# Performance work log

Measured on AMD Instinct MI355X. Metric: run time of the kernel, lower is better.

Reference implementation:

```python
import math
import jax, jax.numpy as jnp
import numpy as np

B, L, N, D = 256, 50, 100000, 128

def _make_pe(max_len, d_model):
    # matches torch PositionalEncoding buffer (sin/cos scaled by 1/1000)
    pe = np.zeros((max_len, d_model), dtype=np.float32)
    position = np.arange(max_len, dtype=np.float32)[:, None]
    div_term = np.exp(np.arange(0, d_model, 2, dtype=np.float32) * (-math.log(10000.0) / d_model))
    pe[:, 0::2] = np.sin(position * div_term) / 1000.0
    pe[:, 1::2] = np.cos(position * div_term) / 1000.0
    return jnp.asarray(pe)

def setup_inputs() -> dict:
    key = jax.random.key(0)
    ks = jax.random.split(key, 8)
    g = 1.414  # xavier gain used in the torch module
    seeds = jax.random.randint(ks[0], (B, L), 0, N)
    labels = jax.random.randint(ks[1], (B,), 0, N)
    E = jax.random.normal(ks[2], (N, D), dtype=jnp.float32) * 0.02
    W1 = jax.random.normal(ks[3], (D, D), dtype=jnp.float32) * (g * math.sqrt(2.0 / (D + D)))
    W2 = jax.random.normal(ks[4], (D, D), dtype=jnp.float32) * (g * math.sqrt(2.0 / (D + D)))
    q = jax.random.normal(ks[5], (D,), dtype=jnp.float32) * (g * math.sqrt(2.0 / (1 + D)))
    b_att = jax.random.normal(ks[6], (1,), dtype=jnp.float32) * 0.01
    out_bias = jax.random.normal(ks[7], (N,), dtype=jnp.float32) * 0.01
    pe = _make_pe(L, D)
    return {"seeds": seeds, "labels": labels, "E": E, "W1": W1, "W2": W2,
            "q": q, "b_att": b_att, "out_bias": out_bias, "pe": pe}

def reference(seeds, labels, E, W1, W2, q, b_att, out_bias, pe):
    # user_representation: gather seed embeddings, add positional encoding (eval mode: dropout is identity)
    v = E[seeds] + pe[None, :, :]                 # (B, L, D)
    vn = v[:, -1, :]                              # (B, D) last element of each seed set
    # SoftAttention: att_i = q @ (W1 @ v_i + W2 @ vn + b); no softmax in original
    inp = jnp.einsum('bld,ed->ble', v, W1) + jnp.einsum('bd,ed->be', vn, W2)[:, None, :] + b_att[0]
    att = jnp.einsum('ble,e->bl', inp, q)         # (B, L) raw attention weights
    u = jnp.einsum('bl,bld->bd', att, v)          # (B, D) user representations
    # scores = F.linear(u, E, out_bias)
    scores = u @ E.T + out_bias                   # (B, N)
    logp = jax.nn.log_softmax(scores, axis=-1)
    base_loss = -jnp.mean(jnp.take_along_axis(logp, labels[:, None], axis=1))
    return scores, base_loss
```

## Files before the change

kernel.cpp:

```cpp
#include <hip/hip_runtime.h>
#include <hip/hip_bf16.h>

#define B_SZ 256
#define L_SZ 50
#define N_SZ 100000
#define D_SZ 128
#define NBT ((N_SZ + 63) / 64)

typedef __attribute__((ext_vector_type(8))) short bf16x8;
typedef __attribute__((ext_vector_type(4))) float f32x4;

__device__ inline unsigned short f2bf(float f) {
    union { float f; unsigned u; } v; v.f = f;
    unsigned r = v.u + 0x7FFFu + ((v.u >> 16) & 1u);
    return (unsigned short)(r >> 16);
}

__global__ __launch_bounds__(128) void k_ub(const int* __restrict__ seeds,
                                            const float* __restrict__ E,
                                            const float* __restrict__ pe,
                                            const float* __restrict__ W1,
                                            const float* __restrict__ W2,
                                            const float* __restrict__ q,
                                            const float* __restrict__ b_att,
                                            unsigned short* __restrict__ u_bf,
                                            float* __restrict__ loss_slot) {
    __shared__ float vbuf[L_SZ][D_SZ + 1];
    __shared__ float att[L_SZ];
    __shared__ float qs[D_SZ], qw1s[D_SZ], qw2s[D_SZ];
    __shared__ float c2s, qsums;
    int b = blockIdx.x, d = threadIdx.x;
    qs[d] = q[d];

    for (int l = 0; l < L_SZ; ++l) {
        int s = seeds[b * L_SZ + l];
        vbuf[l][d] = E[(size_t)s * D_SZ + d] + pe[l * D_SZ + d];
    }
    __syncthreads();

    float a1 = 0.f, a2 = 0.f;
    #pragma unroll 4
    for (int e = 0; e < D_SZ; ++e) {
        float qe = qs[e];
        a1 += qe * W1[e * D_SZ + d];
        a2 += qe * W2[e * D_SZ + d];
    }
    qw1s[d] = a1;
    qw2s[d] = a2;
    __syncthreads();

    if (d < L_SZ) {
        float acc = 0.f;
        #pragma unroll 4
        for (int k = 0; k < D_SZ; ++k) acc += vbuf[d][k] * qw1s[k];
        att[d] = acc;
    } else if (d == L_SZ) {
        float acc = 0.f;
        #pragma unroll 4
        for (int k = 0; k < D_SZ; ++k) acc += vbuf[L_SZ - 1][k] * qw2s[k];
        c2s = acc;
    } else if (d == L_SZ + 1) {
        float s = 0.f;
        for (int i = 0; i < D_SZ; ++i) s += qs[i];
        qsums = s;
    }
    __syncthreads();

    float add = c2s + b_att[0] * qsums;
    float u = 0.f;
    #pragma unroll 5
    for (int l = 0; l < L_SZ; ++l) u += (att[l] + add) * vbuf[l][d];
    u_bf[b * D_SZ + d] = f2bf(u);

    if (b == 0 && d == 0) loss_slot[0] = 0.f;
}

__global__ __launch_bounds__(256, 4) void k_gemm(const float* __restrict__ E,
                                                 const float* __restrict__ out_bias,
                                                 const unsigned short* __restrict__ u_bf,
                                                 float* __restrict__ scores,
                                                 float* __restrict__ partial) {
    __shared__ unsigned short us[128 * D_SZ];
    __shared__ float lds_sum[128];
    int tid = threadIdx.x;
    int w = tid >> 6, lane = tid & 63;
    int tile = blockIdx.x >> 1, hf = blockIdx.x & 1;
    if (tid < 128) lds_sum[tid] = 0.f;

    const char* ub = (const char*)u_bf + hf * 32768;
    #pragma unroll
    for (int r = 0; r < 8; ++r) {
        int off = r * 4096 + tid * 16;
        int b = off >> 8, inrow = off & 255;
        bf16x8 v = *(const bf16x8*)(ub + off);
        *(bf16x8*)((char*)us + b * 256 + (inrow ^ ((b & 7) << 4))) = v;
    }

    int nc = tile * 64 + w * 16;
    bool valid = (nc < N_SZ);
    int lo = lane & 15, hi = lane >> 4;
    int kb = hi * 8;

    long erow = valid ? (nc + lo) : 0;
    bf16x8 efrag[4];
    #pragma unroll
    for (int ks = 0; ks < 4; ++ks) {
        const float* p = E + (size_t)erow * D_SZ + ks * 32 + kb;
        float4 x = *(const float4*)p;
        float4 y = *(const float4*)(p + 4);
        bf16x8 f;
        f[0] = (short)f2bf(x.x); f[1] = (short)f2bf(x.y);
        f[2] = (short)f2bf(x.z); f[3] = (short)f2bf(x.w);
        f[4] = (short)f2bf(y.x); f[5] = (short)f2bf(y.y);
        f[6] = (short)f2bf(y.z); f[7] = (short)f2bf(y.w);
        efrag[ks] = f;
    }
    int nb = valid ? (nc + hi * 4) : 0;
    float4 bias4 = *(const float4*)(out_bias + nb);

    __syncthreads();

    #pragma unroll
    for (int rs = 0; rs < 8; ++rs) {
        f32x4 acc = (f32x4){0.f, 0.f, 0.f, 0.f};
        #pragma unroll
        for (int ks = 0; ks < 4; ++ks) {
            int b = rs * 16 + lo;
            int kcol = ks * 64 + hi * 16;
            bf16x8 uf = *(const bf16x8*)((const char*)us + b * 256 + (kcol ^ ((b & 7) << 4)));
            acc = __builtin_amdgcn_mfma_f32_16x16x32_bf16(efrag[ks], uf, acc, 0, 0, 0);
        }
        int jl = rs * 16 + lo;
        int jr = hf * 128 + jl;
        f32x4 c;
        c[0] = acc[0] + bias4.x;
        c[1] = acc[1] + bias4.y;
        c[2] = acc[2] + bias4.z;
        c[3] = acc[3] + bias4.w;
        if (valid)
            *(f32x4*)(scores + (size_t)jr * N_SZ + nb) = c;
        float p = __expf(c[0]) + __expf(c[1]) + __expf(c[2]) + __expf(c[3]);
        p += __shfl_xor(p, 16);
        p += __shfl_xor(p, 32);
        if (valid && hi == 0) atomicAdd(&lds_sum[jl], p);
    }
    __syncthreads();
    if (tid < 128) partial[(size_t)tile * B_SZ + hf * 128 + tid] = lds_sum[tid];
}

__global__ __launch_bounds__(256) void k_loss(const float* __restrict__ partial,
                                              const float* __restrict__ scores,
                                              const int* __restrict__ labels,
                                              float* __restrict__ out_loss) {
    int b = blockIdx.x, t = threadIdx.x;
    float acc = 0.f;
    for (int i = t; i < NBT; i += 256) acc += partial[(size_t)i * B_SZ + b];
    __shared__ float red[256];
    red[t] = acc;
    __syncthreads();
    for (int s = 128; s > 0; s >>= 1) {
        if (t < s) red[t] += red[t + s];
        __syncthreads();
    }
    if (t == 0) {
        int lab = labels[b];
        float val = scores[(size_t)b * N_SZ + lab] - logf(red[0]);
        atomicAdd(out_loss, -val * (1.0f / (float)B_SZ));
    }
}

extern "C" void kernel_launch(void* const* d_in, const int* in_sizes, int n_in,
                              void* d_out, int out_size, void* d_ws, size_t ws_size,
                              hipStream_t stream) {
    const int*   seeds    = (const int*)d_in[0];
    const int*   labels   = (const int*)d_in[1];
    const float* E        = (const float*)d_in[2];
    const float* W1       = (const float*)d_in[3];
    const float* W2       = (const float*)d_in[4];
    const float* q        = (const float*)d_in[5];
    const float* b_att    = (const float*)d_in[6];
    const float* out_bias = (const float*)d_in[7];
    const float* pe       = (const float*)d_in[8];

    float* scores = (float*)d_out;
    float* loss   = scores + (size_t)B_SZ * N_SZ;

    unsigned short* u_bf    = (unsigned short*)((char*)d_ws + 2048);
    float*          partial = (float*)((char*)d_ws + 67584);

    k_ub<<<B_SZ, 128, 0, stream>>>(seeds, E, pe, W1, W2, q, b_att, u_bf, loss);
    k_gemm<<<NBT * 2, 256, 0, stream>>>(E, out_bias, u_bf, scores, partial);
    k_loss<<<B_SZ, 256, 0, stream>>>(partial, scores, labels, loss);
}
```

Before: 64.82 us.

## Use persistent grid-stride GEMM blocks and widen u-computation kernel to 512 threads

The scores GEMM now launches a fixed 1024 blocks that loop over column tiles, instead of one block per tile. Each block therefore loads and swizzles the 128-row bf16 u slice into LDS once, not once per tile, and the partial-sum buffer shrinks so the loss reduction reads fewer entries. The user-representation kernel goes from 128 to 512 threads: it splits the gather, the q·W projections, the attention dot products and the weighted sum across four groups and reduces with shuffles and LDS. The trade-off is fewer resident waves to hide E-load latency in the GEMM, because each tile's loads are no longer overlapped across separate blocks.

```diff
diff --git a/kernel.cpp b/kernel.cpp
--- a/kernel.cpp
+++ b/kernel.cpp
@@ -6,6 +6,7 @@
 #define N_SZ 100000
 #define D_SZ 128
 #define NBT ((N_SZ + 63) / 64)
+#define NSTREAM 512
 
 typedef __attribute__((ext_vector_type(8))) short bf16x8;
 typedef __attribute__((ext_vector_type(4))) float f32x4;
@@ -16,7 +17,7 @@
     return (unsigned short)(r >> 16);
 }
 
-__global__ __launch_bounds__(128) void k_ub(const int* __restrict__ seeds,
+__global__ __launch_bounds__(512) void k_ub(const int* __restrict__ seeds,
                                             const float* __restrict__ E,
                                             const float* __restrict__ pe,
                                             const float* __restrict__ W1,
@@ -26,53 +27,82 @@
                                             unsigned short* __restrict__ u_bf,
                                             float* __restrict__ loss_slot) {
     __shared__ float vbuf[L_SZ][D_SZ + 1];
+    __shared__ int   sseed[L_SZ];
+    __shared__ float qs[D_SZ], qw1s[D_SZ], qw2s[D_SZ];
+    __shared__ float part1[4][D_SZ], part2[4][D_SZ];
     __shared__ float att[L_SZ];
-    __shared__ float qs[D_SZ], qw1s[D_SZ], qw2s[D_SZ];
     __shared__ float c2s, qsums;
-    int b = blockIdx.x, d = threadIdx.x;
-    qs[d] = q[d];
-
-    for (int l = 0; l < L_SZ; ++l) {
-        int s = seeds[b * L_SZ + l];
-        vbuf[l][d] = E[(size_t)s * D_SZ + d] + pe[l * D_SZ + d];
-    }
-    __syncthreads();
-
-    float a1 = 0.f, a2 = 0.f;
+    int b = blockIdx.x, t = threadIdx.x;
+    int g = t >> 7, d = t & 127;
+
+    if (t < L_SZ) sseed[t] = seeds[b * L_SZ + t];
+    if (t < D_SZ) qs[t] = q[t];
+    __syncthreads();
+
     #pragma unroll 4
-    for (int e = 0; e < D_SZ; ++e) {
-        float qe = qs[e];
-        a1 += qe * W1[e * D_SZ + d];
-        a2 += qe * W2[e * D_SZ + d];
-    }
-    qw1s[d] = a1;
-    qw2s[d] = a2;
-    __syncthreads();
-
-    if (d < L_SZ) {
-        float acc = 0.f;
-        #pragma unroll 4
-        for (int k = 0; k < D_SZ; ++k) acc += vbuf[d][k] * qw1s[k];
-        att[d] = acc;
-    } else if (d == L_SZ) {
-        float acc = 0.f;
-        #pragma unroll 4
-        for (int k = 0; k < D_SZ; ++k) acc += vbuf[L_SZ - 1][k] * qw2s[k];
-        c2s = acc;
-    } else if (d == L_SZ + 1) {
-        float s = 0.f;
-        for (int i = 0; i < D_SZ; ++i) s += qs[i];
-        qsums = s;
+    for (int l = g; l < L_SZ; l += 4)
+        vbuf[l][d] = E[(size_t)sseed[l] * D_SZ + d] + pe[l * D_SZ + d];
+
+    {
+        float a1 = 0.f, a2 = 0.f;
+        int e0 = g * 32;
+        #pragma unroll 8
+        for (int e = e0; e < e0 + 32; ++e) {
+            float qe = qs[e];
+            a1 += qe * W1[e * D_SZ + d];
+            a2 += qe * W2[e * D_SZ + d];
+        }
+        part1[g][d] = a1;
+        part2[g][d] = a2;
+    }
+    __syncthreads();
+    if (t < D_SZ) {
+        qw1s[t] = part1[0][t] + part1[1][t] + part1[2][t] + part1[3][t];
+        qw2s[t] = part2[0][t] + part2[1][t] + part2[2][t] + part2[3][t];
+    }
+    __syncthreads();
+
+    if (t < L_SZ * 8) {
+        int l = t >> 3, sub = t & 7;
+        float p = 0.f;
+        #pragma unroll
+        for (int k = sub * 16; k < sub * 16 + 16; ++k) p += vbuf[l][k] * qw1s[k];
+        p += __shfl_xor(p, 1, 8);
+        p += __shfl_xor(p, 2, 8);
+        p += __shfl_xor(p, 4, 8);
+        if (sub == 0) att[l] = p;
+    } else if (t < L_SZ * 8 + 8) {
+        int sub = t & 7;
+        float p = 0.f;
+        #pragma unroll
+        for (int k = sub * 16; k < sub * 16 + 16; ++k) p += vbuf[L_SZ - 1][k] * qw2s[k];
+        p += __shfl_xor(p, 1, 8);
+        p += __shfl_xor(p, 2, 8);
+        p += __shfl_xor(p, 4, 8);
+        if (sub == 0) c2s = p;
+    } else if (t < L_SZ * 8 + 16) {
+        int sub = t & 7;
+        float p = 0.f;
+        #pragma unroll
+        for (int k = sub * 16; k < sub * 16 + 16; ++k) p += qs[k];
+        p += __shfl_xor(p, 1, 8);
+        p += __shfl_xor(p, 2, 8);
+        p += __shfl_xor(p, 4, 8);
+        if (sub == 0) qsums = p;
     }
     __syncthreads();
 
     float add = c2s + b_att[0] * qsums;
-    float u = 0.f;
-    #pragma unroll 5
-    for (int l = 0; l < L_SZ; ++l) u += (att[l] + add) * vbuf[l][d];
-    u_bf[b * D_SZ + d] = f2bf(u);
-
-    if (b == 0 && d == 0) loss_slot[0] = 0.f;
+    float up = 0.f;
+    #pragma unroll 4
+    for (int l = g; l < L_SZ; l += 4) up += (att[l] + add) * vbuf[l][d];
+    __syncthreads();
+    part1[g][d] = up;
+    __syncthreads();
+    if (t < D_SZ)
+        u_bf[b * D_SZ + t] = f2bf(part1[0][t] + part1[1][t] + part1[2][t] + part1[3][t]);
+
+    if (b == 0 && t == 0) loss_slot[0] = 0.f;
 }
 
 __global__ __launch_bounds__(256, 4) void k_gemm(const float* __restrict__ E,
@@ -84,68 +114,71 @@
     __shared__ float lds_sum[128];
     int tid = threadIdx.x;
     int w = tid >> 6, lane = tid & 63;
-    int tile = blockIdx.x >> 1, hf = blockIdx.x & 1;
+    int s = blockIdx.x >> 1, hf = blockIdx.x & 1;
     if (tid < 128) lds_sum[tid] = 0.f;
 
     const char* ub = (const char*)u_bf + hf * 32768;
     #pragma unroll
     for (int r = 0; r < 8; ++r) {
         int off = r * 4096 + tid * 16;
-        int b = off >> 8, inrow = off & 255;
+        int brow = off >> 8, inrow = off & 255;
         bf16x8 v = *(const bf16x8*)(ub + off);
-        *(bf16x8*)((char*)us + b * 256 + (inrow ^ ((b & 7) << 4))) = v;
-    }
-
-    int nc = tile * 64 + w * 16;
-    bool valid = (nc < N_SZ);
+        *(bf16x8*)((char*)us + brow * 256 + (inrow ^ ((brow & 7) << 4))) = v;
+    }
+
     int lo = lane & 15, hi = lane >> 4;
     int kb = hi * 8;
-
-    long erow = valid ? (nc + lo) : 0;
-    bf16x8 efrag[4];
-    #pragma unroll
-    for (int ks = 0; ks < 4; ++ks) {
-        const float* p = E + (size_t)erow * D_SZ + ks * 32 + kb;
-        float4 x = *(const float4*)p;
-        float4 y = *(const float4*)(p + 4);
-        bf16x8 f;
-        f[0] = (short)f2bf(x.x); f[1] = (short)f2bf(x.y);
-        f[2] = (short)f2bf(x.z); f[3] = (short)f2bf(x.w);
-        f[4] = (short)f2bf(y.x); f[5] = (short)f2bf(y.y);
-        f[6] = (short)f2bf(y.z); f[7] = (short)f2bf(y.w);
-        efrag[ks] = f;
-    }
-    int nb = valid ? (nc + hi * 4) : 0;
-    float4 bias4 = *(const float4*)(out_bias + nb);
-
-    __syncthreads();
-
-    #pragma unroll
-    for (int rs = 0; rs < 8; ++rs) {
-        f32x4 acc = (f32x4){0.f, 0.f, 0.f, 0.f};
+    __syncthreads();
+
+    for (int ct = s; ct < NBT; ct += NSTREAM) {
+        int nc = ct * 64 + w * 16;
+        bool valid = (nc < N_SZ);
+
+        long erow = valid ? (nc + lo) : 0;
+        bf16x8 efrag[4];
         #pragma unroll
         for (int ks = 0; ks < 4; ++ks) {
-            int b = rs * 16 + lo;
-            int kcol = ks * 64 + hi * 16;
-            bf16x8 uf = *(const bf16x8*)((const char*)us + b * 256 + (kcol ^ ((b & 7) << 4)));
-            acc = __builtin_amdgcn_mfma_f32_16x16x32_bf16(efrag[ks], uf, acc, 0, 0, 0);
+            const float* p = E + (size_t)erow * D_SZ + ks * 32 + kb;
+            float4 x = *(const float4*)p;
+            float4 y = *(const float4*)(p + 4);
+            bf16x8 f;
+            f[0] = (short)f2bf(x.x); f[1] = (short)f2bf(x.y);
+            f[2] = (short)f2bf(x.z); f[3] = (short)f2bf(x.w);
+            f[4] = (short)f2bf(y.x); f[5] = (short)f2bf(y.y);
+            f[6] = (short)f2bf(y.z); f[7] = (short)f2bf(y.w);
+            efrag[ks] = f;
         }
-        int jl = rs * 16 + lo;
-        int jr = hf * 128 + jl;
-        f32x4 c;
-        c[0] = acc[0] + bias4.x;
-        c[1] = acc[1] + bias4.y;
-        c[2] = acc[2] + bias4.z;
-        c[3] = acc[3] + bias4.w;
-        if (valid)
-            *(f32x4*)(scores + (size_t)jr * N_SZ + nb) = c;
-        float p = __expf(c[0]) + __expf(c[1]) + __expf(c[2]) + __expf(c[3]);
-        p += __shfl_xor(p, 16);
-        p += __shfl_xor(p, 32);
-        if (valid && hi == 0) atomicAdd(&lds_sum[jl], p);
-    }
-    __syncthreads();
-    if (tid < 128) partial[(size_t)tile * B_SZ + hf * 128 + tid] = lds_sum[tid];
+        int nb = valid ? (nc + hi * 4) : 0;
+        float4 bias4 = *(const float4*)(out_bias + nb);
+
+        #pragma unroll
+        for (int rs = 0; rs < 8; ++rs) {
+            f32x4 acc = (f32x4){0.f, 0.f, 0.f, 0.f};
+            #pragma unroll
+            for (int ks = 0; ks < 4; ++ks) {
+                int brow = rs * 16 + lo;
+                int kcol = ks * 64 + hi * 16;
+                bf16x8 uf = *(const bf16x8*)((const char*)us + brow * 256 + (kcol ^ ((brow & 7) << 4)));
+                acc = __builtin_amdgcn_mfma_f32_16x16x32_bf16(efrag[ks], uf, acc, 0, 0, 0);
+            }
+            int jl = rs * 16 + lo;
+            int jr = hf * 128 + jl;
+            f32x4 c;
+            c[0] = acc[0] + bias4.x;
+            c[1] = acc[1] + bias4.y;
+            c[2] = acc[2] + bias4.z;
+            c[3] = acc[3] + bias4.w;
+            if (valid) {
+                *(f32x4*)(scores + (size_t)jr * N_SZ + nb) = c;
+                float p = __expf(c[0]) + __expf(c[1]) + __expf(c[2]) + __expf(c[3]);
+                p += __shfl_xor(p, 16);
+                p += __shfl_xor(p, 32);
+                if (hi == 0) atomicAdd(&lds_sum[jl], p);
+            }
+        }
+    }
+    __syncthreads();
+    if (tid < 128) partial[(size_t)blockIdx.x * 128 + tid] = lds_sum[tid];
 }
 
 __global__ __launch_bounds__(256) void k_loss(const float* __restrict__ partial,
@@ -153,13 +186,14 @@
                                               const int* __restrict__ labels,
                                               float* __restrict__ out_loss) {
     int b = blockIdx.x, t = threadIdx.x;
+    int hf = b >> 7, r = b & 127;
     float acc = 0.f;
-    for (int i = t; i < NBT; i += 256) acc += partial[(size_t)i * B_SZ + b];
+    for (int i = t; i < NSTREAM; i += 256) acc += partial[(size_t)(i * 2 + hf) * 128 + r];
     __shared__ float red[256];
     red[t] = acc;
     __syncthreads();
-    for (int s = 128; s > 0; s >>= 1) {
-        if (t < s) red[t] += red[t + s];
+    for (int st = 128; st > 0; st >>= 1) {
+        if (t < st) red[t] += red[t + st];
         __syncthreads();
     }
     if (t == 0) {
@@ -188,7 +222,7 @@
     unsigned short* u_bf    = (unsigned short*)((char*)d_ws + 2048);
     float*          partial = (float*)((char*)d_ws + 67584);
 
-    k_ub<<<B_SZ, 128, 0, stream>>>(seeds, E, pe, W1, W2, q, b_att, u_bf, loss);
-    k_gemm<<<NBT * 2, 256, 0, stream>>>(E, out_bias, u_bf, scores, partial);
+    k_ub<<<B_SZ, 512, 0, stream>>>(seeds, E, pe, W1, W2, q, b_att, u_bf, loss);
+    k_gemm<<<NSTREAM * 2, 256, 0, stream>>>(E, out_bias, u_bf, scores, partial);
     k_loss<<<B_SZ, 256, 0, stream>>>(partial, scores, labels, loss);
 }
```

New measurement: 105.5 us. 1.63x slower.
